# Kernel tuning notes

Hardware: AMD Instinct MI355X
Metric: run time of the kernel (lower is better)

Reference implementation:

```python
import jax, jax.numpy as jnp
import numpy as np

B, N, CA, CS, CZ, H, NQ, NK = 2, 16384, 128, 128, 16, 4, 32, 128
DH = CA // H
NB = N // NQ


def _ln(x, gamma=None, eps=1e-5):
    m = jnp.mean(x, -1, keepdims=True)
    v = jnp.var(x, -1, keepdims=True)
    y = (x - m) * jax.lax.rsqrt(v + eps)
    return y if gamma is None else y * gamma


def _adaln(a, s, gamma_s, Wg, bg, Wskip):
    # AF3 Algorithm 26: LN(a) without affine; LN(s) with scale, no offset;
    # out = sigmoid(Linear(s)) * a + LinearNoBias(s)
    a_n = _ln(a)
    s_n = _ln(s, gamma_s)
    return jax.nn.sigmoid(s_n @ Wg + bg) * a_n + s_n @ Wskip


def setup_inputs():
    key = jax.random.key(0)
    ks = jax.random.split(key, 20)
    def nrm(i, shape, scale=0.02):
        return jax.random.normal(ks[i], shape, jnp.float32) * scale
    return {
        "a": jax.random.normal(ks[0], (B, N, CA), jnp.float32),
        "s": jax.random.normal(ks[1], (B, N, CS), jnp.float32),
        "z": jax.random.normal(ks[2], (B, NB, NQ, NK, CZ), jnp.float32),
        "apb_gamma_s": jnp.ones((CS,), jnp.float32),
        "apb_Wg": nrm(3, (CS, CA)),
        "apb_bg": jnp.zeros((CA,), jnp.float32),
        "apb_Wskip": nrm(4, (CS, CA)),
        "Wq": nrm(5, (CA, CA)), "bq": jnp.zeros((CA,), jnp.float32),
        "Wk": nrm(6, (CA, CA)), "Wv": nrm(7, (CA, CA)),
        "Wgate": nrm(8, (CA, CA)), "Wo": nrm(9, (CA, CA)),
        "gamma_z": jnp.ones((CZ,), jnp.float32),
        "Wz": nrm(10, (CZ, H)),
        "Ws_last": nrm(11, (CS, CA)),
        "bs_last": jnp.full((CA,), -2.0, jnp.float32),
        "ct_gamma_s": jnp.ones((CS,), jnp.float32),
        "ct_Wg": nrm(12, (CS, CA)), "ct_bg": jnp.zeros((CA,), jnp.float32),
        "ct_Wskip": nrm(13, (CS, CA)),
        "Wa1": nrm(14, (CA, 2 * CA)), "Wa2": nrm(15, (CA, 2 * CA)),
        "Wb": nrm(16, (2 * CA, CA)),
        "Ws": nrm(17, (CS, CA)), "bs": jnp.full((CA,), -2.0, jnp.float32),
        "n_queries": NQ, "n_keys": NK,
    }


def reference(a, s, z, apb_gamma_s, apb_Wg, apb_bg, apb_Wskip, Wq, bq, Wk, Wv,
              Wgate, Wo, gamma_z, Wz, Ws_last, bs_last, ct_gamma_s, ct_Wg,
              ct_bg, ct_Wskip, Wa1, Wa2, Wb, Ws, bs, n_queries, n_keys):
    nq, nk = int(n_queries), int(n_keys)
    nb = N // nq
    # ---- AttentionPairBias, local windowed attention ----
    a1 = _adaln(a, s, apb_gamma_s, apb_Wg, apb_bg, apb_Wskip)  # [B,N,CA]
    # trunked pair bias: [B,nb,nq,nk,H] -> [B,H,nb,nq,nk]
    bias = jnp.transpose(_ln(z, gamma_z) @ Wz, (0, 4, 1, 2, 3))
    q = (a1 @ Wq + bq).reshape(B, N, H, DH).transpose(0, 2, 1, 3)
    k = (a1 @ Wk).reshape(B, N, H, DH).transpose(0, 2, 1, 3)
    v = (a1 @ Wv).reshape(B, N, H, DH).transpose(0, 2, 1, 3)
    qb = q.reshape(B, H, nb, nq, DH)
    pad = (nk - nq) // 2
    # centered key window per query block
    idx = (jnp.arange(nb) * nq - pad)[:, None] + jnp.arange(nk)[None, :]  # [nb,nk]
    valid = (idx >= 0) & (idx < N)
    idxc = jnp.clip(idx, 0, N - 1)
    kb = k[:, :, idxc]  # [B,H,nb,nk,DH]
    vb = v[:, :, idxc]
    scores = jnp.einsum('bhnqd,bhnkd->bhnqk', qb, kb) / np.sqrt(DH).astype(np.float32) + bias
    scores = jnp.where(valid[None, None, :, None, :], scores, -1e9)
    attn = jax.nn.softmax(scores, axis=-1)
    o = jnp.einsum('bhnqk,bhnkd->bhnqd', attn, vb)  # [B,H,nb,nq,DH]
    o = o.reshape(B, H, N, DH).transpose(0, 2, 1, 3).reshape(B, N, CA)
    g = jax.nn.sigmoid(a1 @ Wgate)  # per-channel gating
    attn_out = (g * o) @ Wo
    b_out = jax.nn.sigmoid(s @ Ws_last + bs_last) * attn_out
    # ---- ConditionedTransitionBlock (Alg 25) ----
    a3 = _adaln(a, s, ct_gamma_s, ct_Wg, ct_bg, ct_Wskip)
    t = jax.nn.silu(a3 @ Wa1) * (a3 @ Wa2)
    ct_out = jax.nn.sigmoid(s @ Ws + bs) * (t @ Wb)
    # Alg 23: a = b + ConditionedTransitionBlock(a, s)
    return b_out + ct_out
```

## Files before the change

kernel.cpp:

```cpp
#include <hip/hip_runtime.h>

typedef _Float16 f16;
typedef f16 f16x8 __attribute__((ext_vector_type(8)));
typedef f16 f16x4 __attribute__((ext_vector_type(4)));
typedef float f32x4 __attribute__((ext_vector_type(4)));

#define MFMA16(a,b,c) __builtin_amdgcn_mfma_f32_16x16x32_f16((a),(b),(c),0,0,0)

static __device__ __forceinline__ f16x8 ld8(const f16* p){ return *(const f16x8*)p; }
static __device__ __forceinline__ float sigm(float x){ return 1.f/(1.f + __expf(-x)); }

__global__ __launch_bounds__(256) void k_prep(
    const float* __restrict__ apb_gamma, const float* __restrict__ apb_Wg, const float* __restrict__ apb_Wskip,
    const float* __restrict__ ct_gamma,  const float* __restrict__ ct_Wg,  const float* __restrict__ ct_Wskip,
    const float* __restrict__ Wq, const float* __restrict__ Wk, const float* __restrict__ Wv, const float* __restrict__ Wgate,
    const float* __restrict__ Wsl, const float* __restrict__ Wss,
    const float* __restrict__ Wa1, const float* __restrict__ Wa2,
    const float* __restrict__ Wo, const float* __restrict__ Wb,
    const float* __restrict__ gamma_z, const float* __restrict__ Wz,
    f16* __restrict__ wA, f16* __restrict__ wC, f16* __restrict__ wQK, f16* __restrict__ wVG,
    f16* __restrict__ wSG, f16* __restrict__ wAB, f16* __restrict__ wO, f16* __restrict__ wBt,
    float* __restrict__ wzg, float* __restrict__ Slv, float* __restrict__ Ssv)
{
  const int t0 = blockIdx.x*256 + threadIdx.x;
  const int stride = gridDim.x*256;
  for (int i = t0; i < 256*128; i += stride){
    const int n = i >> 7, k = i & 127;
    const int m = n & 127;
    wA[i]  = (f16)(((n<128) ? apb_Wg[k*128+m] : apb_Wskip[k*128+m]) * apb_gamma[k]);
    wC[i]  = (f16)(((n<128) ? ct_Wg[k*128+m]  : ct_Wskip[k*128+m])  * ct_gamma[k]);
    wQK[i] = (f16)((n<128) ? Wq[k*128+m] : Wk[k*128+m]);
    wVG[i] = (f16)((n<128) ? Wv[k*128+m] : Wgate[k*128+m]);
    wSG[i] = (f16)((n<128) ? Wsl[k*128+m] : Wss[k*128+m]);
  }
  for (int i = t0; i < 512*128; i += stride){
    const int n = i >> 7, k = i & 127;
    wAB[i] = (f16)((n < 256) ? Wa1[k*256 + n] : Wa2[k*256 + (n-256)]);
  }
  for (int i = t0; i < 128*128; i += stride){
    const int n = i >> 7, k = i & 127;
    wO[i] = (f16)Wo[k*128+n];
  }
  for (int i = t0; i < 128*256; i += stride){
    const int n = i >> 8, k = i & 255;
    wBt[i] = (f16)Wb[k*128+n];
  }
  if (t0 < 64) wzg[t0] = gamma_z[t0 & 15] * Wz[(t0 & 15)*4 + (t0 >> 4)];
  if (t0 < 256){
    const int cc = t0 & 127;
    const float* Wp = (t0 >= 128) ? Wss : Wsl;
    float acc = 0.f;
    for (int k = 0; k < 128; k++) acc += Wp[k*128 + cc];
    if (t0 >= 128) Ssv[cc] = acc; else Slv[cc] = acc;
  }
}

__global__ __launch_bounds__(256, 4) void k_pre(
    const float* __restrict__ A, const float* __restrict__ S,
    const f16* __restrict__ wA, const f16* __restrict__ wC,
    const f16* __restrict__ wQK, const f16* __restrict__ wVG,
    const f16* __restrict__ wSG, const f16* __restrict__ wAB,
    const float* __restrict__ bgA, const float* __restrict__ bgC,
    const float* __restrict__ bq, const float* __restrict__ bsl, const float* __restrict__ bss,
    const float* __restrict__ Slv, const float* __restrict__ Ssv,
    f16* __restrict__ Qo, f16* __restrict__ Ko, f16* __restrict__ Vt, f16* __restrict__ Go,
    f16* __restrict__ T, f16* __restrict__ GL, f16* __restrict__ GS)
{
  __shared__ f16 lsn[32*136];
  __shared__ f16 lan[32*136];
  __shared__ f16 la1[32*136];
  __shared__ float lsm[32], lsd[32];
  const int tid = threadIdx.x;
  const size_t rbase = (size_t)blockIdx.x * 32;

  {
    const int half = tid >> 7;
    const int row = (tid & 127) >> 2, part = tid & 3;
    const size_t gr = rbase + row;
    const float* p = (half ? A : S) + gr*128 + part*32;
    float v[32];
    #pragma unroll
    for (int j = 0; j < 8; j++){
      const float4 t4 = ((const float4*)p)[j];
      v[j*4+0]=t4.x; v[j*4+1]=t4.y; v[j*4+2]=t4.z; v[j*4+3]=t4.w;
    }
    float sm = 0.f, sq = 0.f;
    #pragma unroll
    for (int j = 0; j < 32; j++){ sm += v[j]; sq += v[j]*v[j]; }
    sm += __shfl_xor(sm,1); sq += __shfl_xor(sq,1);
    sm += __shfl_xor(sm,2); sq += __shfl_xor(sq,2);
    const float mean = sm*(1.f/128.f);
    const float var  = sq*(1.f/128.f) - mean*mean;
    const float rstd = rsqrtf(var + 1e-5f);
    if (!half && part == 0){ lsm[row] = mean; lsd[row] = (var + 1e-5f)*rstd; }
    f16* dst = half ? lan : lsn;
    #pragma unroll
    for (int j = 0; j < 4; j++){
      f16x8 o;
      #pragma unroll
      for (int e = 0; e < 8; e++) o[e] = (f16)((v[j*8+e]-mean)*rstd);
      *(f16x8*)&dst[row*136 + part*32 + j*8] = o;
    }
  }
  __syncthreads();

  const int l = tid & 63, w = tid >> 6;
  const int c = l & 15, q4 = l >> 4;

  #pragma unroll
  for (int jj = 0; jj < 2; jj++){
    const int n0 = (jj*4 + w)*16;
    #pragma unroll
    for (int mat = 0; mat < 2; mat++){
      const f16* W = mat ? wC : wA;
      f16x8 b0[4], b1[4];
      #pragma unroll
      for (int kc = 0; kc < 4; kc++){
        b0[kc] = ld8(W + (size_t)(n0 + c)*128 + kc*32 + q4*8);
        b1[kc] = ld8(W + (size_t)(128 + n0 + c)*128 + kc*32 + q4*8);
      }
      const float4 bv = *(const float4*)((mat ? bgC : bgA) + n0 + q4*4);
      const float bvr[4] = {bv.x, bv.y, bv.z, bv.w};
      f16* dst = mat ? lan : la1;
      #pragma unroll
      for (int mi = 0; mi < 2; mi++){
        f32x4 d0 = {0,0,0,0}, d1 = {0,0,0,0};
        #pragma unroll
        for (int kc = 0; kc < 4; kc++){
          const f16x8 av = *(const f16x8*)&lsn[(mi*16 + c)*136 + kc*32 + q4*8];
          d0 = MFMA16(b0[kc], av, d0);
          d1 = MFMA16(b1[kc], av, d1);
        }
        const int row = mi*16 + c;
        const f16x4 anv = *(const f16x4*)&lan[row*136 + n0 + q4*4];
        f16x4 o;
        #pragma unroll
        for (int r = 0; r < 4; r++)
          o[r] = (f16)(sigm(d0[r] + bvr[r])*(float)anv[r] + d1[r]);
        *(f16x4*)&dst[row*136 + n0 + q4*4] = o;
      }
    }
  }
  __syncthreads();

  const int bidx = (int)(rbase >> 14);
  const int ntk0 = (int)(rbase & 16383);

  #pragma unroll
  for (int jj = 0; jj < 2; jj++){
    const int n0 = (jj*4 + w)*16;
    {
      f16x8 bQ[4], bK[4];
      #pragma unroll
      for (int kc = 0; kc < 4; kc++){
        bQ[kc] = ld8(wQK + (size_t)(n0 + c)*128 + kc*32 + q4*8);
        bK[kc] = ld8(wQK + (size_t)(128 + n0 + c)*128 + kc*32 + q4*8);
      }
      const float4 bv = *(const float4*)(bq + n0 + q4*4);
      const float bvr[4] = {bv.x, bv.y, bv.z, bv.w};
      #pragma unroll
      for (int mi = 0; mi < 2; mi++){
        f32x4 dQ = {0,0,0,0}, dK = {0,0,0,0};
        #pragma unroll
        for (int kc = 0; kc < 4; kc++){
          const f16x8 av = *(const f16x8*)&la1[(mi*16 + c)*136 + kc*32 + q4*8];
          dQ = MFMA16(bQ[kc], av, dQ);
          dK = MFMA16(bK[kc], av, dK);
        }
        const size_t grow = rbase + mi*16 + c;
        f16x4 qo, ko;
        #pragma unroll
        for (int r = 0; r < 4; r++){
          qo[r] = (f16)((dQ[r] + bvr[r])*0.17677669529663687f);
          ko[r] = (f16)dK[r];
        }
        *(f16x4*)&Qo[grow*128 + n0 + q4*4] = qo;
        *(f16x4*)&Ko[grow*128 + n0 + q4*4] = ko;
      }
    }
    {
      f16x8 bV[4], bG[4];
      #pragma unroll
      for (int kc = 0; kc < 4; kc++){
        bV[kc] = ld8(wVG + (size_t)(n0 + c)*128 + kc*32 + q4*8);
        bG[kc] = ld8(wVG + (size_t)(128 + n0 + c)*128 + kc*32 + q4*8);
      }
      #pragma unroll
      for (int mi = 0; mi < 2; mi++){
        f32x4 dV = {0,0,0,0}, dG = {0,0,0,0};
        #pragma unroll
        for (int kc = 0; kc < 4; kc++){
          const f16x8 av = *(const f16x8*)&la1[(mi*16 + c)*136 + kc*32 + q4*8];
          dV = MFMA16(av, bV[kc], dV);
          dG = MFMA16(bG[kc], av, dG);
        }
        const size_t grow = rbase + mi*16 + c;
        f16x4 go;
        #pragma unroll
        for (int r = 0; r < 4; r++) go[r] = (f16)sigm(dG[r]);
        *(f16x4*)&Go[grow*128 + n0 + q4*4] = go;
        f16x4 vv;
        #pragma unroll
        for (int r = 0; r < 4; r++) vv[r] = (f16)dV[r];
        *(f16x4*)(Vt + ((size_t)bidx*128 + n0 + c)*16384 + ntk0 + mi*16 + q4*4) = vv;
      }
    }
  }

  #pragma unroll
  for (int jj = 0; jj < 4; jj++){
    const int n0t = (jj*4 + w)*16;
    f16x8 b1v[4], b2v[4];
    #pragma unroll
    for (int kc = 0; kc < 4; kc++){
      b1v[kc] = ld8(wAB + (size_t)(n0t + c)*128 + kc*32 + q4*8);
      b2v[kc] = ld8(wAB + (size_t)(256 + n0t + c)*128 + kc*32 + q4*8);
    }
    #pragma unroll
    for (int mi = 0; mi < 2; mi++){
      f32x4 d0 = {0,0,0,0}, d1 = {0,0,0,0};
      #pragma unroll
      for (int kc = 0; kc < 4; kc++){
        const f16x8 av = *(const f16x8*)&lan[(mi*16 + c)*136 + kc*32 + q4*8];
        d0 = MFMA16(b1v[kc], av, d0);
        d1 = MFMA16(b2v[kc], av, d1);
      }
      const size_t grow = rbase + mi*16 + c;
      f16x4 t4;
      #pragma unroll
      for (int r = 0; r < 4; r++){
        const float u = d0[r];
        t4[r] = (f16)((u*sigm(u))*d1[r]);
      }
      *(f16x4*)&T[grow*256 + n0t + q4*4] = t4;
    }
  }

  #pragma unroll
  for (int jj = 0; jj < 2; jj++){
    const int n0 = (jj*4 + w)*16;
    f16x8 b0[4], b1[4];
    #pragma unroll
    for (int kc = 0; kc < 4; kc++){
      b0[kc] = ld8(wSG + (size_t)(n0 + c)*128 + kc*32 + q4*8);
      b1[kc] = ld8(wSG + (size_t)(128 + n0 + c)*128 + kc*32 + q4*8);
    }
    const float4 sl4 = *(const float4*)(Slv + n0 + q4*4);
    const float4 ss4 = *(const float4*)(Ssv + n0 + q4*4);
    const float4 bl4 = *(const float4*)(bsl + n0 + q4*4);
    const float4 bs4 = *(const float4*)(bss + n0 + q4*4);
    const float slr[4] = {sl4.x,sl4.y,sl4.z,sl4.w};
    const float ssr[4] = {ss4.x,ss4.y,ss4.z,ss4.w};
    const float blr[4] = {bl4.x,bl4.y,bl4.z,bl4.w};
    const float bsr[4] = {bs4.x,bs4.y,bs4.z,bs4.w};
    #pragma unroll
    for (int mi = 0; mi < 2; mi++){
      f32x4 d0 = {0,0,0,0}, d1 = {0,0,0,0};
      #pragma unroll
      for (int kc = 0; kc < 4; kc++){
        const f16x8 av = *(const f16x8*)&lsn[(mi*16 + c)*136 + kc*32 + q4*8];
        d0 = MFMA16(b0[kc], av, d0);
        d1 = MFMA16(b1[kc], av, d1);
      }
      const int row = mi*16 + c;
      const size_t grow = rbase + row;
      const float mn = lsm[row], sd = lsd[row];
      f16x4 gl4, gs4;
      #pragma unroll
      for (int r = 0; r < 4; r++){
        gl4[r] = (f16)sigm(d0[r]*sd + mn*slr[r] + blr[r]);
        gs4[r] = (f16)sigm(d1[r]*sd + mn*ssr[r] + bsr[r]);
      }
      *(f16x4*)&GL[grow*128 + n0 + q4*4] = gl4;
      *(f16x4*)&GS[grow*128 + n0 + q4*4] = gs4;
    }
  }
}

__global__ __launch_bounds__(512) void k_attn(const f16* __restrict__ Q, const f16* __restrict__ K,
    const f16* __restrict__ VT, const float* __restrict__ Z, const float* __restrict__ WZG,
    f16* __restrict__ Og)
{
  __shared__ f16 upb[17408];
  __shared__ float wzg_s[64];
  const int tid = threadIdx.x;
  const int b = blockIdx.x >> 9, nb = blockIdx.x & 511;
  if (tid < 64) wzg_s[tid] = WZG[tid];
  __syncthreads();
  #pragma unroll
  for (int i = 0; i < 8; i++){
    const int p  = tid + i*512;
    const int qq = p >> 7, kk = p & 127;
    const float* zp = Z + ((((size_t)b*512 + nb)*32 + qq)*128 + kk)*16;
    const float4 z0 = *(const float4*)(zp);
    const float4 z1 = *(const float4*)(zp + 4);
    const float4 z2 = *(const float4*)(zp + 8);
    const float4 z3 = *(const float4*)(zp + 12);
    const float xs[16] = {z0.x,z0.y,z0.z,z0.w, z1.x,z1.y,z1.z,z1.w,
                          z2.x,z2.y,z2.z,z2.w, z3.x,z3.y,z3.z,z3.w};
    float sm = 0.f, sq = 0.f;
    #pragma unroll
    for (int cc = 0; cc < 16; cc++){ sm += xs[cc]; sq += xs[cc]*xs[cc]; }
    const float mean = sm*(1.f/16.f);
    const float var  = sq*(1.f/16.f) - mean*mean;
    const float rs   = rsqrtf(var + 1e-5f);
    #pragma unroll
    for (int h = 0; h < 4; h++){
      float acc = 0.f;
      #pragma unroll
      for (int cc = 0; cc < 16; cc++) acc += (xs[cc]-mean)*wzg_s[h*16+cc];
      upb[(h*32 + qq)*132 + kk] = (f16)(acc*rs);
    }
  }
  __syncthreads();

  const int l = tid & 63, w = tid >> 6;
  const int c = l & 15, q4 = l >> 4;
  const int h = w >> 1, qh = w & 1, m0 = qh*16;
  const f16x8 qf = ld8(Q + ((size_t)b*16384 + (size_t)nb*32 + m0 + c)*128 + h*32 + q4*8);
  const long kbase = (long)b*16384 + (long)nb*32 - 48;
  f32x4 sc[8];
  #pragma unroll
  for (int nt = 0; nt < 8; nt++){
    const f16x8 kf = ld8(K + (kbase + nt*16 + c)*128 + h*32 + q4*8);
    f32x4 zz = {0.f,0.f,0.f,0.f};
    sc[nt] = MFMA16(kf, qf, zz);
  }
  #pragma unroll
  for (int nt = 0; nt < 8; nt++){
    const f16x4 bb = *(const f16x4*)&upb[(h*32 + m0 + c)*132 + nt*16 + q4*4];
    #pragma unroll
    for (int r = 0; r < 4; r++){
      const long kt = (long)nb*32 - 48 + nt*16 + q4*4 + r;
      const bool inv = (kt < 0) || (kt >= 16384);
      sc[nt][r] = inv ? -1e9f : (sc[nt][r] + (float)bb[r]);
    }
  }
  float mx = sc[0][0];
  #pragma unroll
  for (int nt = 0; nt < 8; nt++)
    #pragma unroll
    for (int r = 0; r < 4; r++) mx = fmaxf(mx, sc[nt][r]);
  mx = fmaxf(mx, __shfl_xor(mx, 16));
  mx = fmaxf(mx, __shfl_xor(mx, 32));
  float sum = 0.f;
  #pragma unroll
  for (int nt = 0; nt < 8; nt++)
    #pragma unroll
    for (int r = 0; r < 4; r++){ const float e = __expf(sc[nt][r]-mx); sc[nt][r] = e; sum += e; }
  sum += __shfl_xor(sum, 16);
  sum += __shfl_xor(sum, 32);
  const float inv = 1.f/sum;
  __syncthreads();
  #pragma unroll
  for (int nt = 0; nt < 8; nt++){
    f16x4 p4;
    #pragma unroll
    for (int r = 0; r < 4; r++) p4[r] = (f16)(sc[nt][r]*inv);
    *(f16x4*)&upb[(w*16 + c)*136 + nt*16 + q4*4] = p4;
  }
  const f16* vb = VT + ((long)b*128)*16384 + (long)nb*32 - 48;
  f32x4 o0 = {0.f,0.f,0.f,0.f}, o1 = {0.f,0.f,0.f,0.f};
  #pragma unroll
  for (int kc = 0; kc < 4; kc++){
    const f16x8 pa = *(const f16x8*)&upb[(w*16 + c)*136 + kc*32 + q4*8];
    const f16x8 v0 = ld8(vb + (long)(h*32 + c)*16384 + kc*32 + q4*8);
    const f16x8 v1 = ld8(vb + (long)(h*32 + 16 + c)*16384 + kc*32 + q4*8);
    o0 = MFMA16(pa, v0, o0);
    o1 = MFMA16(pa, v1, o1);
  }
  #pragma unroll
  for (int r = 0; r < 4; r++){
    const size_t tok = (size_t)b*16384 + (size_t)nb*32 + m0 + q4*4 + r;
    Og[tok*128 + h*32 + c]      = (f16)o0[r];
    Og[tok*128 + h*32 + 16 + c] = (f16)o1[r];
  }
}

__global__ __launch_bounds__(256, 4) void k_final(const f16* __restrict__ G, const f16* __restrict__ O,
    const f16* __restrict__ T, const f16* __restrict__ Wot, const f16* __restrict__ Wbt,
    const f16* __restrict__ GL, const f16* __restrict__ GS, float* __restrict__ out)
{
  const int l = threadIdx.x & 63, w = threadIdx.x >> 6;
  const int c = l & 15, q4 = l >> 4;
  const int rh = w & 1, ch = w >> 1;
  const size_t mrow = (size_t)blockIdx.x*32 + rh*16 + c;
  f16x8 ag[4], at[8];
  const f16* gp = G + mrow*128 + q4*8;
  const f16* op = O + mrow*128 + q4*8;
  #pragma unroll
  for (int kc = 0; kc < 4; kc++) ag[kc] = ld8(gp + kc*32) * ld8(op + kc*32);
  const f16* tp = T + mrow*256 + q4*8;
  #pragma unroll
  for (int kc = 0; kc < 8; kc++) at[kc] = ld8(tp + kc*32);
  #pragma unroll
  for (int ntl = 0; ntl < 4; ntl++){
    const int cb = (ch*4 + ntl)*16;
    f32x4 d1 = {0,0,0,0}, d2 = {0,0,0,0};
    #pragma unroll
    for (int kc = 0; kc < 4; kc++)
      d1 = MFMA16(ld8(Wot + (size_t)(cb + c)*128 + kc*32 + q4*8), ag[kc], d1);
    #pragma unroll
    for (int kc = 0; kc < 8; kc++)
      d2 = MFMA16(ld8(Wbt + (size_t)(cb + c)*256 + kc*32 + q4*8), at[kc], d2);
    const f16x4 glv = *(const f16x4*)&GL[mrow*128 + cb + q4*4];
    const f16x4 gsv = *(const f16x4*)&GS[mrow*128 + cb + q4*4];
    float4 o;
    o.x = (float)glv[0]*d1[0] + (float)gsv[0]*d2[0];
    o.y = (float)glv[1]*d1[1] + (float)gsv[1]*d2[1];
    o.z = (float)glv[2]*d1[2] + (float)gsv[2]*d2[2];
    o.w = (float)glv[3]*d1[3] + (float)gsv[3]*d2[3];
    *(float4*)&out[mrow*128 + cb + q4*4] = o;
  }
}

extern "C" void kernel_launch(void* const* d_in, const int* in_sizes, int n_in,
                              void* d_out, int out_size, void* d_ws, size_t ws_size,
                              hipStream_t stream)
{
  (void)in_sizes; (void)n_in; (void)out_size; (void)ws_size;
  const float* a        = (const float*)d_in[0];
  const float* s        = (const float*)d_in[1];
  const float* z        = (const float*)d_in[2];
  const float* apb_gamma= (const float*)d_in[3];
  const float* apb_Wg   = (const float*)d_in[4];
  const float* apb_bg   = (const float*)d_in[5];
  const float* apb_Wskip= (const float*)d_in[6];
  const float* Wq       = (const float*)d_in[7];
  const float* bq       = (const float*)d_in[8];
  const float* Wk       = (const float*)d_in[9];
  const float* Wv       = (const float*)d_in[10];
  const float* Wgate    = (const float*)d_in[11];
  const float* Wo       = (const float*)d_in[12];
  const float* gamma_z  = (const float*)d_in[13];
  const float* Wz       = (const float*)d_in[14];
  const float* Wsl      = (const float*)d_in[15];
  const float* bsl      = (const float*)d_in[16];
  const float* ct_gamma = (const float*)d_in[17];
  const float* ct_Wg    = (const float*)d_in[18];
  const float* ct_bg    = (const float*)d_in[19];
  const float* ct_Wskip = (const float*)d_in[20];
  const float* Wa1      = (const float*)d_in[21];
  const float* Wa2      = (const float*)d_in[22];
  const float* Wb       = (const float*)d_in[23];
  const float* Wss      = (const float*)d_in[24];
  const float* bss      = (const float*)d_in[25];

  f16* W0 = (f16*)d_ws;
  const size_t SL = (size_t)32768*128;
  f16* qv = W0 + 0*SL;
  f16* kv = W0 + 1*SL;
  f16* vt = W0 + 2*SL;
  f16* gv = W0 + 3*SL;
  f16* tv = W0 + 4*SL;
  f16* gl = W0 + 6*SL;
  f16* gs = W0 + 7*SL;
  f16* ov = W0 + 8*SL;
  f16* wA  = W0 + 9*SL;
  f16* wC  = wA  + 256*128;
  f16* wQK = wC  + 256*128;
  f16* wVG = wQK + 256*128;
  f16* wSG = wVG + 256*128;
  f16* wAB = wSG + 256*128;
  f16* wO  = wAB + 512*128;
  f16* wBt = wO  + 128*128;
  float* wzg = (float*)(wBt + 128*256);
  float* Slv = wzg + 64;
  float* Ssv = Slv + 128;

  k_prep<<<dim3(64),256,0,stream>>>(apb_gamma,apb_Wg,apb_Wskip, ct_gamma,ct_Wg,ct_Wskip,
      Wq,Wk,Wv,Wgate, Wsl,Wss, Wa1,Wa2, Wo,Wb, gamma_z,Wz,
      wA,wC,wQK,wVG,wSG,wAB,wO,wBt,wzg,Slv,Ssv);
  k_pre<<<dim3(1024),256,0,stream>>>(a,s, wA,wC,wQK,wVG,wSG,wAB,
      apb_bg,ct_bg,bq,bsl,bss,Slv,Ssv, qv,kv,vt,gv,tv,gl,gs);
  k_attn<<<dim3(1024),512,0,stream>>>(qv,kv,vt,z,wzg,ov);
  k_final<<<dim3(1024),256,0,stream>>>(gv,ov,tv,wO,wBt,gl,gs,(float*)d_out);
}
```

Baseline: 555.9 us.

## Fuse final projection into attention kernel and parallelize column-sum prep

Merges the final output projection (gated attention output times Wo plus transition times Wb, with sigmoid gates) into the attention kernel. The attention output tile stays in shared memory instead of going through a global buffer, which removes one kernel launch and one round trip of the O tensor. The prep kernel's column-sum reduction is also split across four lanes with shuffle reductions, and its grid is doubled. In exchange the attention kernel's epilogue grows, which may raise register pressure and lower occupancy.

```diff
diff --git a/kernel.cpp b/kernel.cpp
--- a/kernel.cpp
+++ b/kernel.cpp
@@ -46,12 +46,17 @@
     wBt[i] = (f16)Wb[k*128+n];
   }
   if (t0 < 64) wzg[t0] = gamma_z[t0 & 15] * Wz[(t0 & 15)*4 + (t0 >> 4)];
-  if (t0 < 256){
-    const int cc = t0 & 127;
-    const float* Wp = (t0 >= 128) ? Wss : Wsl;
+  if (t0 < 1024){
+    const int mat = t0 >> 9;
+    const int j = t0 & 511;
+    const int cc = j >> 2, part = j & 3;
+    const float* Wp = mat ? Wss : Wsl;
     float acc = 0.f;
-    for (int k = 0; k < 128; k++) acc += Wp[k*128 + cc];
-    if (t0 >= 128) Ssv[cc] = acc; else Slv[cc] = acc;
+    #pragma unroll 4
+    for (int k = part*32; k < part*32 + 32; k++) acc += Wp[k*128 + cc];
+    acc += __shfl_xor(acc, 1);
+    acc += __shfl_xor(acc, 2);
+    if (part == 0){ if (mat) Ssv[cc] = acc; else Slv[cc] = acc; }
   }
 }
 
@@ -279,7 +284,9 @@
 
 __global__ __launch_bounds__(512) void k_attn(const f16* __restrict__ Q, const f16* __restrict__ K,
     const f16* __restrict__ VT, const float* __restrict__ Z, const float* __restrict__ WZG,
-    f16* __restrict__ Og)
+    const f16* __restrict__ Go, const f16* __restrict__ T,
+    const f16* __restrict__ Wot, const f16* __restrict__ Wbt,
+    const f16* __restrict__ GL, const f16* __restrict__ GS, float* __restrict__ out)
 {
   __shared__ f16 upb[17408];
   __shared__ float wzg_s[64];
@@ -369,48 +376,37 @@
     o0 = MFMA16(pa, v0, o0);
     o1 = MFMA16(pa, v1, o1);
   }
+  __syncthreads();
   #pragma unroll
   for (int r = 0; r < 4; r++){
-    const size_t tok = (size_t)b*16384 + (size_t)nb*32 + m0 + q4*4 + r;
-    Og[tok*128 + h*32 + c]      = (f16)o0[r];
-    Og[tok*128 + h*32 + 16 + c] = (f16)o1[r];
-  }
-}
-
-__global__ __launch_bounds__(256, 4) void k_final(const f16* __restrict__ G, const f16* __restrict__ O,
-    const f16* __restrict__ T, const f16* __restrict__ Wot, const f16* __restrict__ Wbt,
-    const f16* __restrict__ GL, const f16* __restrict__ GS, float* __restrict__ out)
-{
-  const int l = threadIdx.x & 63, w = threadIdx.x >> 6;
-  const int c = l & 15, q4 = l >> 4;
-  const int rh = w & 1, ch = w >> 1;
-  const size_t mrow = (size_t)blockIdx.x*32 + rh*16 + c;
-  f16x8 ag[4], at[8];
-  const f16* gp = G + mrow*128 + q4*8;
-  const f16* op = O + mrow*128 + q4*8;
-  #pragma unroll
-  for (int kc = 0; kc < 4; kc++) ag[kc] = ld8(gp + kc*32) * ld8(op + kc*32);
-  const f16* tp = T + mrow*256 + q4*8;
-  #pragma unroll
-  for (int kc = 0; kc < 8; kc++) at[kc] = ld8(tp + kc*32);
-  #pragma unroll
-  for (int ntl = 0; ntl < 4; ntl++){
-    const int cb = (ch*4 + ntl)*16;
+    upb[(m0 + q4*4 + r)*140 + h*32 + c]      = (f16)o0[r];
+    upb[(m0 + q4*4 + r)*140 + h*32 + 16 + c] = (f16)o1[r];
+  }
+  __syncthreads();
+
+  const size_t tb = (size_t)b*16384 + (size_t)nb*32;
+  #pragma unroll
+  for (int mi = 0; mi < 2; mi++){
+    const size_t tok = tb + mi*16 + c;
     f32x4 d1 = {0,0,0,0}, d2 = {0,0,0,0};
     #pragma unroll
-    for (int kc = 0; kc < 4; kc++)
-      d1 = MFMA16(ld8(Wot + (size_t)(cb + c)*128 + kc*32 + q4*8), ag[kc], d1);
+    for (int kc = 0; kc < 4; kc++){
+      const f16x8 gof = ld8(Go + tok*128 + kc*32 + q4*8) *
+                        *(const f16x8*)&upb[(mi*16 + c)*140 + kc*32 + q4*8];
+      d1 = MFMA16(ld8(Wot + (size_t)(w*16 + c)*128 + kc*32 + q4*8), gof, d1);
+    }
     #pragma unroll
     for (int kc = 0; kc < 8; kc++)
-      d2 = MFMA16(ld8(Wbt + (size_t)(cb + c)*256 + kc*32 + q4*8), at[kc], d2);
-    const f16x4 glv = *(const f16x4*)&GL[mrow*128 + cb + q4*4];
-    const f16x4 gsv = *(const f16x4*)&GS[mrow*128 + cb + q4*4];
+      d2 = MFMA16(ld8(Wbt + (size_t)(w*16 + c)*256 + kc*32 + q4*8),
+                  ld8(T + tok*256 + kc*32 + q4*8), d2);
+    const f16x4 glv = *(const f16x4*)&GL[tok*128 + w*16 + q4*4];
+    const f16x4 gsv = *(const f16x4*)&GS[tok*128 + w*16 + q4*4];
     float4 o;
     o.x = (float)glv[0]*d1[0] + (float)gsv[0]*d2[0];
     o.y = (float)glv[1]*d1[1] + (float)gsv[1]*d2[1];
     o.z = (float)glv[2]*d1[2] + (float)gsv[2]*d2[2];
     o.w = (float)glv[3]*d1[3] + (float)gsv[3]*d2[3];
-    *(float4*)&out[mrow*128 + cb + q4*4] = o;
+    *(float4*)&out[tok*128 + w*16 + q4*4] = o;
   }
 }
 
@@ -455,8 +451,7 @@
   f16* tv = W0 + 4*SL;
   f16* gl = W0 + 6*SL;
   f16* gs = W0 + 7*SL;
-  f16* ov = W0 + 8*SL;
-  f16* wA  = W0 + 9*SL;
+  f16* wA  = W0 + 8*SL;
   f16* wC  = wA  + 256*128;
   f16* wQK = wC  + 256*128;
   f16* wVG = wQK + 256*128;
@@ -468,11 +463,10 @@
   float* Slv = wzg + 64;
   float* Ssv = Slv + 128;
 
-  k_prep<<<dim3(64),256,0,stream>>>(apb_gamma,apb_Wg,apb_Wskip, ct_gamma,ct_Wg,ct_Wskip,
+  k_prep<<<dim3(128),256,0,stream>>>(apb_gamma,apb_Wg,apb_Wskip, ct_gamma,ct_Wg,ct_Wskip,
       Wq,Wk,Wv,Wgate, Wsl,Wss, Wa1,Wa2, Wo,Wb, gamma_z,Wz,
       wA,wC,wQK,wVG,wSG,wAB,wO,wBt,wzg,Slv,Ssv);
   k_pre<<<dim3(1024),256,0,stream>>>(a,s, wA,wC,wQK,wVG,wSG,wAB,
       apb_bg,ct_bg,bq,bsl,bss,Slv,Ssv, qv,kv,vt,gv,tv,gl,gs);
-  k_attn<<<dim3(1024),512,0,stream>>>(qv,kv,vt,z,wzg,ov);
-  k_final<<<dim3(1024),256,0,stream>>>(gv,ov,tv,wO,wBt,gl,gs,(float*)d_out);
+  k_attn<<<dim3(1024),512,0,stream>>>(qv,kv,vt,z,wzg, gv,tv,wO,wBt,gl,gs,(float*)d_out);
 }
```

After: 558.1 us. About the same (+0.4%).
